# Kernel tuning notes

Measured on AMD Instinct MI355X. Metric: run time of the kernel, lower is better.

## Reference

```python
import jax, jax.numpy as jnp
import numpy as np

NCA_HIDDEN = 16
N_CODES = 32
EMBED_DIM = 64


def conv2d(x, w, pad, b=None):
    # x: (N, Cin, H, W), w: (Cout, Cin, kh, kw)
    y = jax.lax.conv_general_dilated(
        x, w, window_strides=(1, 1), padding=[(pad, pad), (pad, pad)],
        dimension_numbers=('NCHW', 'OIHW', 'NCHW'))
    if b is not None:
        y = y + b[None, :, None, None]
    return y


def setup_inputs() -> dict:
    key = jax.random.key(0)
    ks = jax.random.split(key, 32)
    rn = lambda k, shp, s=0.05: jax.random.normal(k, shp, dtype=jnp.float32) * s
    H = NCA_HIDDEN
    upd = H * H * 3 * 3  # 2304
    tau = H * H          # 256
    inp = {
        'demo_inputs':  jax.random.normal(ks[0], (8, 1, 64, 64), dtype=jnp.float32),
        'demo_outputs': jax.random.normal(ks[1], (8, 1, 64, 64), dtype=jnp.float32),
        'test_input':   jax.random.normal(ks[2], (16, 1, 256, 256), dtype=jnp.float32),
        # TaskEncoder params
        'enc_w1': rn(ks[3], (16, 2, 3, 3)),  'enc_b1': jnp.zeros((16,), jnp.float32),
        'enc_w2': rn(ks[4], (32, 16, 3, 3)), 'enc_b2': jnp.zeros((32,), jnp.float32),
        'enc_lw': rn(ks[5], (EMBED_DIM, 32)), 'enc_lb': jnp.zeros((EMBED_DIM,), jnp.float32),
        # gen_update hypernet
        'gu_w1': rn(ks[6], (128, EMBED_DIM)), 'gu_b1': jnp.zeros((128,), jnp.float32),
        'gu_w2': rn(ks[7], (upd, 128)),       'gu_b2': jnp.zeros((upd,), jnp.float32),
        # gen_tau hypernet
        'gt_w1': rn(ks[8], (64, EMBED_DIM)),  'gt_b1': jnp.zeros((64,), jnp.float32),
        'gt_w2': rn(ks[9], (tau, 64)),        'gt_b2': jnp.zeros((tau,), jnp.float32),
        # stem
        'stem_w': rn(ks[10], (H, 1, 3, 3)), 'stem_b': jnp.zeros((H,), jnp.float32),
        # VQ codebook, init U(-1/n_codes, 1/n_codes)
        'codebook': jax.random.uniform(ks[11], (N_CODES, H), jnp.float32,
                                       minval=-1.0 / N_CODES, maxval=1.0 / N_CODES),
        # decoder 1x1 conv
        'dec_w': rn(ks[12], (1, H, 1, 1)), 'dec_b': jnp.zeros((1,), jnp.float32),
        'n_steps': 5,
    }
    return inp


def reference(demo_inputs, demo_outputs, test_input,
              enc_w1, enc_b1, enc_w2, enc_b2, enc_lw, enc_lb,
              gu_w1, gu_b1, gu_w2, gu_b2,
              gt_w1, gt_b1, gt_w2, gt_b2,
              stem_w, stem_b, codebook, dec_w, dec_b, n_steps):
    H = NCA_HIDDEN
    # --- Task encoder: mean task embedding over demo pairs ---
    pairs = jnp.concatenate([demo_inputs, demo_outputs], axis=1)  # (N,2,h,w)
    h = jax.nn.relu(conv2d(pairs, enc_w1, 1, enc_b1))
    h = jax.nn.relu(conv2d(h, enc_w2, 1, enc_b2))
    h = h.mean(axis=(2, 3))                   # AdaptiveAvgPool2d(1)+Flatten -> (N,32)
    te = (h @ enc_lw.T + enc_lb).mean(axis=0)  # (embed_dim,)
    # --- Hypernetworks generate NCA weights ---
    W_update = (jax.nn.relu(te @ gu_w1.T + gu_b1) @ gu_w2.T + gu_b2).reshape(H, H, 3, 3)
    W_tau = (jax.nn.relu(te @ gt_w1.T + gt_b1) @ gt_w2.T + gt_b2).reshape(H, H, 1, 1)
    # --- Stem ---
    state = jax.nn.relu(conv2d(test_input, stem_w, 1, stem_b))  # (B,16,Hh,Ww)
    cb_sq = (codebook ** 2).sum(axis=1)  # (n_codes,)
    for _ in range(int(n_steps)):
        delta = jax.nn.relu(conv2d(state, W_update, 1))
        beta = jax.nn.sigmoid(conv2d(state, W_tau, 0))
        state = beta * state + (1.0 - beta) * delta
        # --- VQ step (straight-through) ---
        B, C, Hh, Ww = state.shape
        zf = state.transpose(0, 2, 3, 1).reshape(-1, C)  # (B*Hh*Ww, C)
        dists = (zf ** 2).sum(1, keepdims=True) + cb_sq - 2.0 * (zf @ codebook.T)
        idx = jnp.argmin(dists, axis=1)
        zq = codebook[idx].reshape(B, Hh, Ww, C).transpose(0, 3, 1, 2)
        state = state + jax.lax.stop_gradient(zq - state)
    output = jax.nn.sigmoid(conv2d(state, dec_w, 0, dec_b))
    return output
```

## Files before the change

kernel.cpp:

```cpp
#include <hip/hip_runtime.h>
#include <stdint.h>

#define NPIX 65536
#define NIMG 16

typedef float4 F4;
typedef _Float16 h2v __attribute__((ext_vector_type(2)));
typedef _Float16 h8v __attribute__((ext_vector_type(8)));
typedef float    f4v __attribute__((ext_vector_type(4)));

union H8 { h8v v; h2v p[4]; _Float16 e[8]; };

__device__ __forceinline__ float sigm(float x){ return 1.0f/(1.0f+__expf(-x)); }

#if defined(__has_builtin)
#if __has_builtin(__builtin_amdgcn_rcpf)
#define FRCP(x) __builtin_amdgcn_rcpf(x)
#endif
#endif
#ifndef FRCP
#define FRCP(x) (1.0f/(x))
#endif
__device__ __forceinline__ float sigmf(float x){ return FRCP(1.0f + __expf(-x)); }

__device__ __forceinline__ h2v pkrtz(float a, float b){
  return __builtin_bit_cast(h2v, __builtin_amdgcn_cvt_pkrtz(a,b));
}

#if defined(__has_builtin)
#if __has_builtin(__builtin_amdgcn_fdot2)
#define FDOT2(a,b,c) __builtin_amdgcn_fdot2((a),(b),(c),false)
#endif
#endif
#ifndef FDOT2
#define FDOT2(a,b,c) ((c) + (float)(a)[0]*(float)(b)[0] + (float)(a)[1]*(float)(b)[1])
#endif

__global__ __launch_bounds__(256) void k_prep(
    const float* __restrict__ w2, _Float16* __restrict__ wfragE)
{
  int t=threadIdx.x;
  for(int i=t;i<5120;i+=256){
    int j=i&7, rest=i>>3, lane=rest&63, rest2=rest>>6, ks=rest2%5, b=rest2/5;
    int g=lane>>4, nn=lane&15;
    int k=32*ks+8*g+j;
    float v=0.f;
    if(k<144){
      int tap=2*ks+(g>>1), ci=8*(g&1)+j, co=b*16+nn;
      v=w2[co*144+ci*9+tap];
    }
    wfragE[i]=(_Float16)v;
  }
}

__global__ __launch_bounds__(256) void k_enc(
    const float* __restrict__ din, const float* __restrict__ dou,
    const float* __restrict__ w1, const float* __restrict__ b1,
    const float* __restrict__ b2,
    const _Float16* __restrict__ wfragE,
    float* __restrict__ pooled)
{
  __shared__ float2 in_s[400];
  __shared__ h8v st_h[324*3];
  __shared__ float red[4][32];
  __shared__ h2v stwp_s[144];
  __shared__ h2v stbp_s[8];

  const int tid=threadIdx.x;
  const int bx=blockIdx.x, by=blockIdx.y, n=blockIdx.z;
  const float* i0 = din + n*4096;
  const float* i1 = dou + n*4096;

  for(int i=tid;i<400;i+=256){
    int sy=i/20, sx=i-sy*20;
    int gy=by*16-2+sy, gx=bx*16-2+sx;
    bool ok=((unsigned)gy<64u && (unsigned)gx<64u);
    in_s[i] = ok ? make_float2(i0[gy*64+gx], i1[gy*64+gx]) : make_float2(0.f,0.f);
  }
  if(tid<144){
    int q=tid/18, r=tid-18*q;
    stwp_s[tid]=pkrtz(w1[36*q+r], w1[36*q+18+r]);
  } else if(tid<152){
    int q=tid-144;
    stbp_s[q]=pkrtz(b1[2*q], b1[2*q+1]);
  }

  const int lane=tid&63, w=tid>>6, g=lane>>4, nn=lane&15;
  h8v B0[5], B1[5];
  const h8v* wfE=(const h8v*)wfragE;
  #pragma unroll
  for(int ks=0;ks<5;ks++){ B0[ks]=wfE[ks*64+lane]; B1[ks]=wfE[(5+ks)*64+lane]; }
  float b2a=b2[nn], b2b=b2[nn+16];
  __syncthreads();

  for(int p=tid;p<324;p+=256){
    int syh=p/18, sxh=p-syh*18;
    int gy=by*16-1+syh, gx=bx*16-1+sxh;
    H8 o0,o1;
    if((unsigned)gy<64u && (unsigned)gx<64u){
      h2v a2[8];
      #pragma unroll
      for(int q=0;q<8;q++) a2[q]=stbp_s[q];
      #pragma unroll
      for(int ky=0;ky<3;ky++){
        #pragma unroll
        for(int kx=0;kx<3;kx++){
          int tp=ky*3+kx;
          float2 v=in_s[(syh+ky)*20+(sxh+kx)];
          h2v v0=pkrtz(v.x,v.x), v1=pkrtz(v.y,v.y);
          #pragma unroll
          for(int q=0;q<8;q++){
            a2[q]=stwp_s[(2*q)*9+tp]*v0 + a2[q];
            a2[q]=stwp_s[(2*q+1)*9+tp]*v1 + a2[q];
          }
        }
      }
      o0.p[0]=a2[0]; o0.p[1]=a2[1]; o0.p[2]=a2[2]; o0.p[3]=a2[3];
      o1.p[0]=a2[4]; o1.p[1]=a2[5]; o1.p[2]=a2[6]; o1.p[3]=a2[7];
      #pragma unroll
      for(int c=0;c<8;c++){
        o0.e[c]=o0.e[c]>(_Float16)0?o0.e[c]:(_Float16)0;
        o1.e[c]=o1.e[c]>(_Float16)0?o1.e[c]:(_Float16)0;
      }
    } else {
      o0.v=(h8v){0,0,0,0,0,0,0,0};
      o1.v=(h8v){0,0,0,0,0,0,0,0};
    }
    st_h[p*3]  =o0.v;
    st_h[p*3+1]=o1.v;
  }
  __syncthreads();

  f4v acc0[4], acc1[4];
  #pragma unroll
  for(int m=0;m<4;m++){ acc0[m]=(f4v){0.f,0.f,0.f,0.f}; acc1[m]=(f4v){0.f,0.f,0.f,0.f}; }
  #pragma unroll
  for(int ks=0;ks<5;ks++){
    int t=2*ks+(g>>1); if(t>8) t=8;
    int tyo=(t*11)>>5, txo=t-tyo*3;
    int sel=g&1;
    #pragma unroll
    for(int m=0;m<4;m++){
      int sy=4*w+m+tyo;
      h8v a=st_h[(sy*18+nn+txo)*3+sel];
      acc0[m]=__builtin_amdgcn_mfma_f32_16x16x32_f16(a,B0[ks],acc0[m],0,0,0);
      acc1[m]=__builtin_amdgcn_mfma_f32_16x16x32_f16(a,B1[ks],acc1[m],0,0,0);
    }
  }
  float s0=0.f, s1=0.f;
  #pragma unroll
  for(int m=0;m<4;m++)
    #pragma unroll
    for(int r=0;r<4;r++){
      s0+=fmaxf(acc0[m][r]+b2a,0.f);
      s1+=fmaxf(acc1[m][r]+b2b,0.f);
    }
  s0+=__shfl_down(s0,32,64); s0+=__shfl_down(s0,16,64);
  s1+=__shfl_down(s1,32,64); s1+=__shfl_down(s1,16,64);
  if(lane<16){ red[w][nn]=s0; red[w][nn+16]=s1; }
  __syncthreads();
  if(tid<32){
    float s=red[0][tid]+red[1][tid]+red[2][tid]+red[3][tid];
    atomicAdd(&pooled[n*32+tid], s);
  }
}

__global__ __launch_bounds__(256) void k_hyperA(
    const float* __restrict__ pooled,
    const float* __restrict__ lw, const float* __restrict__ lb,
    const float* __restrict__ guw1, const float* __restrict__ gub1,
    const float* __restrict__ gtw1, const float* __restrict__ gtb1,
    const float* __restrict__ gtw2, const float* __restrict__ gtb2,
    const float* __restrict__ cb, const float* __restrict__ decw, const float* __restrict__ decb,
    float* __restrict__ hid_g,
    _Float16* __restrict__ wfrag_g,
    _Float16* __restrict__ Mh_g,
    _Float16* __restrict__ bcb_g, _Float16* __restrict__ omb_g,
    _Float16* __restrict__ cbh_g,
    float* __restrict__ chs_g, float* __restrict__ dvals_g)
{
  __shared__ float hm[32], te_s[64], hid_s[128], hidt_s[64];
  __shared__ float wt_s[256];
  __shared__ float cb_s[512];
  int t = threadIdx.x;
  for(int i=t;i<2560;i+=256) ((unsigned int*)wfrag_g)[i]=0u;
  for(int i=t;i<2508;i+=256) ((unsigned int*)Mh_g)[i]=0u;
  if(t<32){
    float s=0.f;
    for(int n=0;n<8;n++) s += pooled[n*32+t];
    hm[t] = s * (1.0f/32768.0f);
  }
  for(int i=t;i<512;i+=256) cb_s[i]=cb[i];
  __syncthreads();
  if(t<64){
    float s=lb[t];
    for(int c=0;c<32;c++) s = fmaf(lw[t*32+c], hm[c], s);
    te_s[t]=s;
  }
  __syncthreads();
  if(t<128){
    float s=gub1[t];
    for(int j=0;j<64;j++) s = fmaf(guw1[t*64+j], te_s[j], s);
    s=fmaxf(s,0.f);
    hid_s[t]=s; hid_g[t]=s;
  } else if(t<192){
    int i=t-128;
    float s=gtb1[i];
    for(int j=0;j<64;j++) s = fmaf(gtw1[i*64+j], te_s[j], s);
    hidt_s[i]=fmaxf(s,0.f);
  }
  __syncthreads();
  {
    float s=gtb2[t];
    for(int i=0;i<64;i++) s = fmaf(gtw2[t*64+i], hidt_s[i], s);
    int co=t>>4, ci=t&15;
    wt_s[ci*16+co]=s;
  }
  __syncthreads();
  {
    int ci=t>>4, co=t&15;
    int g=ci>>3, j=ci&7, lane=(g<<4)|co;
    wfrag_g[(448+lane)*8+j]=(_Float16)wt_s[ci*16+co];
  }
  for(int o=t;o<512;o+=256){
    int k=o>>4, c=o&15;
    float T=0.f;
    for(int ci=0;ci<16;ci++) T = fmaf(wt_s[ci*16+c], cb_s[k*16+ci], T);
    float beta=sigm(T);
    bcb_g[o]=(_Float16)(beta*cb_s[o]);
    omb_g[o]=(_Float16)(1.f-beta);
    cbh_g[o]=(_Float16)cb_s[o];
  }
  if(t<32){
    float sq=0.f, d=0.f;
    for(int c=0;c<16;c++){ float v=cb_s[t*16+c]; sq=fmaf(v,v,sq); d=fmaf(decw[c],v,d); }
    chs_g[t]=0.5f*sq;
    dvals_g[t]=sigm(d+decb[0]);
  }
}

__global__ __launch_bounds__(256) void k_hyperB(
    const float* __restrict__ guw2, const float* __restrict__ gub2,
    const float* __restrict__ hid_g, const float* __restrict__ cb,
    _Float16* __restrict__ wfrag_g, _Float16* __restrict__ Mh_g)
{
  __shared__ float hid_s[128];
  __shared__ float wu_s[256];
  __shared__ float cb_s[512];
  const int t=threadIdx.x, tp=blockIdx.x;
  if(t<128) hid_s[t]=hid_g[t];
  for(int i=t;i<512;i+=256) cb_s[i]=cb[i];
  __syncthreads();
  const int ci=t>>4, co=t&15;
  const int o=co*144+ci*9+tp;
  float s=gub2[o];
  const F4* gp=(const F4*)(guw2+(size_t)o*128);
  #pragma unroll
  for(int i=0;i<32;i++){
    F4 g=gp[i];
    s=fmaf(g.x,hid_s[4*i],s); s=fmaf(g.y,hid_s[4*i+1],s);
    s=fmaf(g.z,hid_s[4*i+2],s); s=fmaf(g.w,hid_s[4*i+3],s);
  }
  wu_s[ci*16+co]=s;
  {
    int k=tp*16+ci;
    int ks=k>>5, rem=k&31, g2=rem>>3, j=rem&7, lane=(g2<<4)|co;
    wfrag_g[(ks*64+lane)*8+j]=(_Float16)s;
  }
  __syncthreads();
  for(int o2=t;o2<512;o2+=256){
    int k=o2>>4, c=o2&15;
    float m=0.f;
    for(int c2=0;c2<16;c2++) m=fmaf(wu_s[c2*16+c], cb_s[k*16+c2], m);
    Mh_g[k*152+tp*16+c]=(_Float16)m;
  }
}

#define ST_STRIDE 3
struct S1P1 { h8v st[324*ST_STRIDE]; float in[400]; };
union S1U { S1P1 p; unsigned int dt[256*20]; };

__global__ __launch_bounds__(256) void k_step1(
    const float* __restrict__ tin,
    const float* __restrict__ stw, const float* __restrict__ stb,
    const _Float16* __restrict__ wfrag,
    const _Float16* __restrict__ cbh, const float* __restrict__ chs,
    uint8_t* __restrict__ idx_out)
{
  __shared__ S1U u;
  __shared__ h8v cb8_s[64];
  __shared__ float chs_s[32];
  __shared__ h2v stwp_s[72];
  __shared__ h2v stbp_s[8];

  const int tid=threadIdx.x;
  const int bx=blockIdx.x, by=blockIdx.y, n=blockIdx.z;
  const float* in = tin + (size_t)n*NPIX;

  for(int i=tid;i<400;i+=256){
    int sy=i/20, sx=i-sy*20;
    int gy=by*16-2+sy, gx=bx*16-2+sx;
    u.p.in[i] = ((unsigned)gy<256u && (unsigned)gx<256u) ? in[gy*256+gx] : 0.0f;
  }
  if(tid<72){
    int q=tid/9, tp=tid-q*9;
    stwp_s[q*9+tp]=pkrtz(stw[(2*q)*9+tp], stw[(2*q+1)*9+tp]);
  } else if(tid<80){
    int q=tid-72;
    stbp_s[q]=pkrtz(stb[2*q], stb[2*q+1]);
  } else if(tid>=160 && tid<192) chs_s[tid-160]=chs[tid-160];
  if(tid<64) ((uint4*)cb8_s)[tid] = ((const uint4*)cbh)[tid];

  const int lane = tid & 63, w = tid >> 6;
  const int g = lane >> 4, nn = lane & 15;
  h8v Bd[5], Bt2;
  const h8v* wf = (const h8v*)wfrag;
  #pragma unroll
  for(int ks=0;ks<5;ks++) Bd[ks]=wf[ks*64+lane];
  Bt2 = wf[7*64+lane];

  __syncthreads();

  for(int p=tid;p<324;p+=256){
    int syh=p/18, sxh=p-syh*18;
    int gy=by*16-1+syh, gx=bx*16-1+sxh;
    H8 b0,b1;
    if((unsigned)gy<256u && (unsigned)gx<256u){
      h2v a2[8];
      #pragma unroll
      for(int q=0;q<8;q++) a2[q]=stbp_s[q];
      #pragma unroll
      for(int ky=0;ky<3;ky++){
        #pragma unroll
        for(int kx=0;kx<3;kx++){
          int tp=ky*3+kx;
          float v=u.p.in[(syh+ky)*20+(sxh+kx)];
          h2v vv=pkrtz(v,v);
          #pragma unroll
          for(int q=0;q<8;q++) a2[q] = stwp_s[q*9+tp]*vv + a2[q];
        }
      }
      b0.p[0]=a2[0]; b0.p[1]=a2[1]; b0.p[2]=a2[2]; b0.p[3]=a2[3];
      b1.p[0]=a2[4]; b1.p[1]=a2[5]; b1.p[2]=a2[6]; b1.p[3]=a2[7];
      #pragma unroll
      for(int c=0;c<8;c++){
        b0.e[c]=b0.e[c]>(_Float16)0?b0.e[c]:(_Float16)0;
        b1.e[c]=b1.e[c]>(_Float16)0?b1.e[c]:(_Float16)0;
      }
    } else {
      b0.v=(h8v){0,0,0,0,0,0,0,0};
      b1.v=(h8v){0,0,0,0,0,0,0,0};
    }
    u.p.st[p*ST_STRIDE]  =b0.v;
    u.p.st[p*ST_STRIDE+1]=b1.v;
  }
  __syncthreads();

  f4v accd[4], acct[4];
  #pragma unroll
  for(int m=0;m<4;m++){ accd[m]=(f4v){0.f,0.f,0.f,0.f}; acct[m]=(f4v){0.f,0.f,0.f,0.f}; }
  #pragma unroll
  for(int ks=0;ks<5;ks++){
    int t = 2*ks + (g>>1); if(t>8) t=8;
    int tyo=(t*11)>>5, txo=t-tyo*3;
    int sel = g&1;
    #pragma unroll
    for(int m=0;m<4;m++){
      int sy = 4*w+m+tyo;
      h8v a = u.p.st[(sy*18 + nn + txo)*ST_STRIDE + sel];
      accd[m]=__builtin_amdgcn_mfma_f32_16x16x32_f16(a,Bd[ks],accd[m],0,0,0);
      if(ks==2) acct[m]=__builtin_amdgcn_mfma_f32_16x16x32_f16(a,Bt2,acct[m],0,0,0);
    }
  }
  const int py=tid>>4, pxx=tid&15;
  const int cpx=((py+1)*18+pxx+1)*ST_STRIDE;
  h8v z0=u.p.st[cpx], z1=u.p.st[cpx+1];
  __syncthreads();

  #pragma unroll
  for(int m=0;m<4;m++){
    #pragma unroll
    for(int r=0;r<4;r++){
      int px=(4*w+m)*16 + g*4 + r;
      h2v pk = pkrtz(accd[m][r], acct[m][r]);
      u.dt[px*20+nn] = __builtin_bit_cast(unsigned int, pk);
    }
  }
  __syncthreads();

  const uint4* dr=(const uint4*)(u.dt+tid*20);
  uint4 q0=dr[0],q1=dr[1],q2=dr[2],q3=dr[3];
  unsigned int qq[16]={q0.x,q0.y,q0.z,q0.w,q1.x,q1.y,q1.z,q1.w,
                       q2.x,q2.y,q2.z,q2.w,q3.x,q3.y,q3.z,q3.w};
  float zn[16];
  #pragma unroll
  for(int c=0;c<16;c++){
    h2v dt2=__builtin_bit_cast(h2v, qq[c]);
    float d=(float)dt2[0]; d = d>0.f?d:0.f;
    float beta=sigmf((float)dt2[1]);
    float zv = (c<8)? (float)z0[c] : (float)z1[c-8];
    zn[c]=fmaf(beta, zv-d, d);
  }
  H8 u0,u1;
  #pragma unroll
  for(int j=0;j<4;j++){
    u0.p[j]=pkrtz(zn[2*j],zn[2*j+1]);
    u1.p[j]=pkrtz(zn[8+2*j],zn[9+2*j]);
  }
  int best=0; float bv=-3.4e38f;
  #pragma unroll
  for(int k=0;k<32;k++){
    H8 c0,c1; c0.v=cb8_s[k*2]; c1.v=cb8_s[k*2+1];
    float dot=0.f;
    #pragma unroll
    for(int j=0;j<4;j++) dot=FDOT2(u0.p[j],c0.p[j],dot);
    #pragma unroll
    for(int j=0;j<4;j++) dot=FDOT2(u1.p[j],c1.p[j],dot);
    float val=dot-chs_s[k];
    if(val>bv){bv=val;best=k;}
  }
  idx_out[(size_t)n*NPIX + (by*16+py)*256 + (bx*16+pxx)]=(uint8_t)best;
}

__global__ __launch_bounds__(256) void k_stepN(
    const uint8_t* __restrict__ idx_in,
    const uint4* __restrict__ Mh,
    const _Float16* __restrict__ bcbh, const _Float16* __restrict__ ombh,
    const _Float16* __restrict__ cbh,  const float* __restrict__ chs,
    const float* __restrict__ dvals,
    uint8_t* __restrict__ idx_out, float* __restrict__ out, int last)
{
  __shared__ int id_s[18*34];
  __shared__ uint4 M_s[627];
  __shared__ h8v bcb_s[64], omb_s[64], cb8_s[64];
  __shared__ float chs_s[32], dv_s[32];
  const int tid=threadIdx.x;
  const int bx=blockIdx.x, by=blockIdx.y, n=blockIdx.z;
  const uint8_t* ip = idx_in + (size_t)n*NPIX;

  for(int i=tid;i<612;i+=256){
    int sy=i/34, sx=i-sy*34;
    int gy=by*16-1+sy, gx=bx*32-1+sx;
    id_s[i] = ((unsigned)gy<256u && (unsigned)gx<256u) ? (int)ip[gy*256+gx] : 32;
  }
  for(int i=tid;i<627;i+=256) M_s[i]=Mh[i];
  if(tid<64)        ((uint4*)bcb_s)[tid]     = ((const uint4*)bcbh)[tid];
  else if(tid<128)  ((uint4*)omb_s)[tid-64]  = ((const uint4*)ombh)[tid-64];
  else if(tid<192)  ((uint4*)cb8_s)[tid-128] = ((const uint4*)cbh)[tid-128];
  else if(tid<224)  chs_s[tid-192]=chs[tid-192];
  else              dv_s[tid-224]=dvals[tid-224];
  __syncthreads();

  const int r=tid>>4, c0=tid&15;
  const h8v* Mv=(const h8v*)M_s;

  h8v a0A={0,0,0,0,0,0,0,0}, a1A={0,0,0,0,0,0,0,0};
  h8v a0B={0,0,0,0,0,0,0,0}, a1B={0,0,0,0,0,0,0,0};
  int kcA=0, kcB=0;
  #pragma unroll
  for(int dy=0;dy<3;dy++){
    #pragma unroll
    for(int dx=0;dx<3;dx++){
      int t=dy*3+dx;
      int iA=id_s[(r+dy)*34 + c0+dx];
      int iB=id_s[(r+dy)*34 + c0+16+dx];
      if(t==4){ kcA=iA; kcB=iB; }
      const h8v* mA=&Mv[iA*19+t*2];
      const h8v* mB=&Mv[iB*19+t*2];
      a0A+=mA[0]; a1A+=mA[1];
      a0B+=mB[0]; a1B+=mB[1];
    }
  }
  h8v r0A,r1A,r0B,r1B;
  #pragma unroll
  for(int q=0;q<8;q++){
    r0A[q]=a0A[q]>(_Float16)0?a0A[q]:(_Float16)0;
    r1A[q]=a1A[q]>(_Float16)0?a1A[q]:(_Float16)0;
    r0B[q]=a0B[q]>(_Float16)0?a0B[q]:(_Float16)0;
    r1B[q]=a1B[q]>(_Float16)0?a1B[q]:(_Float16)0;
  }
  H8 u0A,u1A,u0B,u1B;
  u0A.v = bcb_s[kcA*2]   + omb_s[kcA*2]  *r0A;
  u1A.v = bcb_s[kcA*2+1] + omb_s[kcA*2+1]*r1A;
  u0B.v = bcb_s[kcB*2]   + omb_s[kcB*2]  *r0B;
  u1B.v = bcb_s[kcB*2+1] + omb_s[kcB*2+1]*r1B;

  int bestA=0,bestB=0; float bvA=-3.4e38f,bvB=-3.4e38f;
  #pragma unroll
  for(int k=0;k<32;k++){
    H8 c0v,c1v; c0v.v=cb8_s[k*2]; c1v.v=cb8_s[k*2+1];
    float ch=chs_s[k];
    float dA=0.f, dB=0.f;
    #pragma unroll
    for(int j=0;j<4;j++){ dA=FDOT2(u0A.p[j],c0v.p[j],dA); dB=FDOT2(u0B.p[j],c0v.p[j],dB); }
    #pragma unroll
    for(int j=0;j<4;j++){ dA=FDOT2(u1A.p[j],c1v.p[j],dA); dB=FDOT2(u1B.p[j],c1v.p[j],dB); }
    float vA=dA-ch, vB=dB-ch;
    if(vA>bvA){bvA=vA;bestA=k;}
    if(vB>bvB){bvB=vB;bestB=k;}
  }
  size_t gidx=(size_t)n*NPIX + (size_t)(by*16+r)*256 + bx*32+c0;
  if(last){ out[gidx]=dv_s[bestA]; out[gidx+16]=dv_s[bestB]; }
  else    { idx_out[gidx]=(uint8_t)bestA; idx_out[gidx+16]=(uint8_t)bestB; }
}

extern "C" void kernel_launch(void* const* d_in, const int* in_sizes, int n_in,
                              void* d_out, int out_size, void* d_ws, size_t ws_size,
                              hipStream_t stream)
{
  const float* demo_in  = (const float*)d_in[0];
  const float* demo_out = (const float*)d_in[1];
  const float* test_in  = (const float*)d_in[2];
  const float* enc_w1 = (const float*)d_in[3];
  const float* enc_b1 = (const float*)d_in[4];
  const float* enc_w2 = (const float*)d_in[5];
  const float* enc_b2 = (const float*)d_in[6];
  const float* enc_lw = (const float*)d_in[7];
  const float* enc_lb = (const float*)d_in[8];
  const float* gu_w1 = (const float*)d_in[9];
  const float* gu_b1 = (const float*)d_in[10];
  const float* gu_w2 = (const float*)d_in[11];
  const float* gu_b2 = (const float*)d_in[12];
  const float* gt_w1 = (const float*)d_in[13];
  const float* gt_b1 = (const float*)d_in[14];
  const float* gt_w2 = (const float*)d_in[15];
  const float* gt_b2 = (const float*)d_in[16];
  const float* stem_w = (const float*)d_in[17];
  const float* stem_b = (const float*)d_in[18];
  const float* codebook = (const float*)d_in[19];
  const float* dec_w = (const float*)d_in[20];
  const float* dec_b = (const float*)d_in[21];

  float* ws = (float*)d_ws;
  float* pooled = ws;
  float* chs    = pooled + 256;
  float* dvals  = chs + 32;
  float* hid_g  = dvals + 32;
  _Float16* hbase = (_Float16*)(ws + 448);
  _Float16* wfrag  = hbase;
  _Float16* wfragE = hbase + 5120;
  _Float16* Mh     = hbase + 10240;
  _Float16* bcbh   = hbase + 15264;
  _Float16* ombh   = hbase + 15776;
  _Float16* cbh    = hbase + 16288;
  uint8_t* idxA = (uint8_t*)(hbase + 16800);
  uint8_t* idxB = idxA + (size_t)NIMG*NPIX;

  (void)hipMemsetAsync(pooled, 0, 256*sizeof(float), stream);
  k_prep<<<1,256,0,stream>>>(enc_w2, wfragE);
  k_enc<<<dim3(4,4,8),256,0,stream>>>(demo_in, demo_out, enc_w1, enc_b1, enc_b2, wfragE, pooled);
  k_hyperA<<<1,256,0,stream>>>(pooled, enc_lw, enc_lb,
                               gu_w1,gu_b1, gt_w1,gt_b1, gt_w2,gt_b2,
                               codebook, dec_w, dec_b,
                               hid_g, wfrag, Mh, bcbh, ombh, cbh, chs, dvals);
  k_hyperB<<<9,256,0,stream>>>(gu_w2, gu_b2, hid_g, codebook, wfrag, Mh);
  dim3 tgrid(16,16,NIMG);
  k_step1<<<tgrid,256,0,stream>>>(test_in, stem_w, stem_b, wfrag, cbh, chs, idxA);
  float* outp = (float*)d_out;
  dim3 sgrid(8,16,NIMG);
  k_stepN<<<sgrid,256,0,stream>>>(idxA,(const uint4*)Mh,bcbh,ombh,cbh,chs,dvals, idxB,outp,0);
  k_stepN<<<sgrid,256,0,stream>>>(idxB,(const uint4*)Mh,bcbh,ombh,cbh,chs,dvals, idxA,outp,0);
  k_stepN<<<sgrid,256,0,stream>>>(idxA,(const uint4*)Mh,bcbh,ombh,cbh,chs,dvals, idxB,outp,0);
  k_stepN<<<sgrid,256,0,stream>>>(idxB,(const uint4*)Mh,bcbh,ombh,cbh,chs,dvals, idxA,outp,1);
}
```

Measured before the change: 248.7 us.

## Process four adjacent pixels per thread in stepN with larger 32x32 tiles

The stepN kernel now covers a 32x32 pixel tile per block, with each thread handling four horizontally adjacent pixels instead of two pixels 16 apart. Each thread loads a 3x6 window of code indices into registers once and reuses it across the four pixels. Output is written as one packed 32-bit word of indices or one float4. The goal is fewer redundant LDS index reads and halo loads, plus wider global stores. In exchange, register pressure rises from more accumulators and the grid is halved to 1024 blocks, which lowers parallelism.

```diff
diff --git a/kernel.cpp b/kernel.cpp
--- a/kernel.cpp
+++ b/kernel.cpp
@@ -430,7 +430,7 @@
     const float* __restrict__ dvals,
     uint8_t* __restrict__ idx_out, float* __restrict__ out, int last)
 {
-  __shared__ int id_s[18*34];
+  __shared__ int id_s[34*34];
   __shared__ uint4 M_s[627];
   __shared__ h8v bcb_s[64], omb_s[64], cb8_s[64];
   __shared__ float chs_s[32], dv_s[32];
@@ -438,9 +438,9 @@
   const int bx=blockIdx.x, by=blockIdx.y, n=blockIdx.z;
   const uint8_t* ip = idx_in + (size_t)n*NPIX;
 
-  for(int i=tid;i<612;i+=256){
+  for(int i=tid;i<1156;i+=256){
     int sy=i/34, sx=i-sy*34;
-    int gy=by*16-1+sy, gx=bx*32-1+sx;
+    int gy=by*32-1+sy, gx=bx*32-1+sx;
     id_s[i] = ((unsigned)gy<256u && (unsigned)gx<256u) ? (int)ip[gy*256+gx] : 32;
   }
   for(int i=tid;i<627;i+=256) M_s[i]=Mh[i];
@@ -451,57 +451,75 @@
   else              dv_s[tid-224]=dvals[tid-224];
   __syncthreads();
 
-  const int r=tid>>4, c0=tid&15;
+  const int r = tid>>3, c0 = (tid&7)*4;
+  int idl[3][6];
+  #pragma unroll
+  for(int dy=0;dy<3;dy++){
+    const int2* rp=(const int2*)&id_s[(r+dy)*34 + c0];
+    int2 e0=rp[0], e1=rp[1], e2=rp[2];
+    idl[dy][0]=e0.x; idl[dy][1]=e0.y; idl[dy][2]=e1.x;
+    idl[dy][3]=e1.y; idl[dy][4]=e2.x; idl[dy][5]=e2.y;
+  }
+
   const h8v* Mv=(const h8v*)M_s;
-
-  h8v a0A={0,0,0,0,0,0,0,0}, a1A={0,0,0,0,0,0,0,0};
-  h8v a0B={0,0,0,0,0,0,0,0}, a1B={0,0,0,0,0,0,0,0};
-  int kcA=0, kcB=0;
+  h8v a0[4], a1[4];
+  #pragma unroll
+  for(int j=0;j<4;j++){ a0[j]=(h8v){0,0,0,0,0,0,0,0}; a1[j]=(h8v){0,0,0,0,0,0,0,0}; }
   #pragma unroll
   for(int dy=0;dy<3;dy++){
     #pragma unroll
     for(int dx=0;dx<3;dx++){
       int t=dy*3+dx;
-      int iA=id_s[(r+dy)*34 + c0+dx];
-      int iB=id_s[(r+dy)*34 + c0+16+dx];
-      if(t==4){ kcA=iA; kcB=iB; }
-      const h8v* mA=&Mv[iA*19+t*2];
-      const h8v* mB=&Mv[iB*19+t*2];
-      a0A+=mA[0]; a1A+=mA[1];
-      a0B+=mB[0]; a1B+=mB[1];
-    }
-  }
-  h8v r0A,r1A,r0B,r1B;
-  #pragma unroll
-  for(int q=0;q<8;q++){
-    r0A[q]=a0A[q]>(_Float16)0?a0A[q]:(_Float16)0;
-    r1A[q]=a1A[q]>(_Float16)0?a1A[q]:(_Float16)0;
-    r0B[q]=a0B[q]>(_Float16)0?a0B[q]:(_Float16)0;
-    r1B[q]=a1B[q]>(_Float16)0?a1B[q]:(_Float16)0;
-  }
-  H8 u0A,u1A,u0B,u1B;
-  u0A.v = bcb_s[kcA*2]   + omb_s[kcA*2]  *r0A;
-  u1A.v = bcb_s[kcA*2+1] + omb_s[kcA*2+1]*r1A;
-  u0B.v = bcb_s[kcB*2]   + omb_s[kcB*2]  *r0B;
-  u1B.v = bcb_s[kcB*2+1] + omb_s[kcB*2+1]*r1B;
-
-  int bestA=0,bestB=0; float bvA=-3.4e38f,bvB=-3.4e38f;
+      #pragma unroll
+      for(int j=0;j<4;j++){
+        int kk=idl[dy][dx+j];
+        const h8v* mp=&Mv[kk*19+t*2];
+        a0[j]+=mp[0]; a1[j]+=mp[1];
+      }
+    }
+  }
+
+  H8 u0[4], u1[4];
+  #pragma unroll
+  for(int j=0;j<4;j++){
+    int kc=idl[1][j+1];
+    h8v r0,r1;
+    #pragma unroll
+    for(int q=0;q<8;q++){
+      r0[q]=a0[j][q]>(_Float16)0?a0[j][q]:(_Float16)0;
+      r1[q]=a1[j][q]>(_Float16)0?a1[j][q]:(_Float16)0;
+    }
+    u0[j].v = bcb_s[kc*2]   + omb_s[kc*2]  *r0;
+    u1[j].v = bcb_s[kc*2+1] + omb_s[kc*2+1]*r1;
+  }
+
+  float bv[4]={-3.4e38f,-3.4e38f,-3.4e38f,-3.4e38f};
+  int best[4]={0,0,0,0};
   #pragma unroll
   for(int k=0;k<32;k++){
     H8 c0v,c1v; c0v.v=cb8_s[k*2]; c1v.v=cb8_s[k*2+1];
     float ch=chs_s[k];
-    float dA=0.f, dB=0.f;
-    #pragma unroll
-    for(int j=0;j<4;j++){ dA=FDOT2(u0A.p[j],c0v.p[j],dA); dB=FDOT2(u0B.p[j],c0v.p[j],dB); }
-    #pragma unroll
-    for(int j=0;j<4;j++){ dA=FDOT2(u1A.p[j],c1v.p[j],dA); dB=FDOT2(u1B.p[j],c1v.p[j],dB); }
-    float vA=dA-ch, vB=dB-ch;
-    if(vA>bvA){bvA=vA;bestA=k;}
-    if(vB>bvB){bvB=vB;bestB=k;}
-  }
-  size_t gidx=(size_t)n*NPIX + (size_t)(by*16+r)*256 + bx*32+c0;
-  if(last){ out[gidx]=dv_s[bestA]; out[gidx+16]=dv_s[bestB]; }
-  else    { idx_out[gidx]=(uint8_t)bestA; idx_out[gidx+16]=(uint8_t)bestB; }
+    #pragma unroll
+    for(int j=0;j<4;j++){
+      float dot=0.f;
+      #pragma unroll
+      for(int q=0;q<4;q++) dot=FDOT2(u0[j].p[q],c0v.p[q],dot);
+      #pragma unroll
+      for(int q=0;q<4;q++) dot=FDOT2(u1[j].p[q],c1v.p[q],dot);
+      float val=dot-ch;
+      if(val>bv[j]){bv[j]=val;best[j]=k;}
+    }
+  }
+
+  size_t gbase=(size_t)n*NPIX + (size_t)(by*32+r)*256 + bx*32+c0;
+  if(last){
+    float4 o=make_float4(dv_s[best[0]],dv_s[best[1]],dv_s[best[2]],dv_s[best[3]]);
+    *(float4*)(out+gbase)=o;
+  } else {
+    unsigned int pk=(unsigned)best[0] | ((unsigned)best[1]<<8)
+                  | ((unsigned)best[2]<<16) | ((unsigned)best[3]<<24);
+    *(unsigned int*)(idx_out+gbase)=pk;
+  }
 }
 
 extern "C" void kernel_launch(void* const* d_in, const int* in_sizes, int n_in,
@@ -557,7 +575,7 @@
   dim3 tgrid(16,16,NIMG);
   k_step1<<<tgrid,256,0,stream>>>(test_in, stem_w, stem_b, wfrag, cbh, chs, idxA);
   float* outp = (float*)d_out;
-  dim3 sgrid(8,16,NIMG);
+  dim3 sgrid(8,8,NIMG);
   k_stepN<<<sgrid,256,0,stream>>>(idxA,(const uint4*)Mh,bcbh,ombh,cbh,chs,dvals, idxB,outp,0);
   k_stepN<<<sgrid,256,0,stream>>>(idxB,(const uint4*)Mh,bcbh,ombh,cbh,chs,dvals, idxA,outp,0);
   k_stepN<<<sgrid,256,0,stream>>>(idxA,(const uint4*)Mh,bcbh,ombh,cbh,chs,dvals, idxB,outp,0);
```

After: 256.2 us. +3.0%, slower.
